# Kernel optimization log

Hardware: AMD Instinct MI355X
Metric: run time of the kernel (lower is better)

The kernel has to match this reference:

```python
import jax, jax.numpy as jnp
import numpy as np

B, S, HID = 2, 2048, 4096
NH, NKV, HD = 32, 8, 128
SLIDING_WINDOW = 1024
ROPE_THETA = 10000.0


def setup_inputs() -> dict:
    key = jax.random.key(0)
    ks = jax.random.split(key, 6)
    hidden_states = jax.random.normal(ks[0], (B, S, HID), dtype=jnp.float32)
    attention_mask = jnp.ones((B, S), dtype=jnp.int32)
    position_ids = jnp.broadcast_to(jnp.arange(S, dtype=jnp.int32)[None, :], (B, S))
    sc = 1.0 / np.sqrt(HID)
    q_w = jax.random.normal(ks[1], (HID, NH * HD), dtype=jnp.float32) * sc
    k_w = jax.random.normal(ks[2], (HID, NKV * HD), dtype=jnp.float32) * sc
    v_w = jax.random.normal(ks[3], (HID, NKV * HD), dtype=jnp.float32) * sc
    o_w = jax.random.normal(ks[4], (NH * HD, HID), dtype=jnp.float32) * sc
    return {"hidden_states": hidden_states, "attention_mask": attention_mask,
            "position_ids": position_ids, "q_w": q_w, "k_w": k_w, "v_w": v_w, "o_w": o_w}


def _rotate_half(x):
    return jnp.concatenate((-x[..., x.shape[-1] // 2:], x[..., : x.shape[-1] // 2]), axis=-1)


def _rope_sincos(position_ids):
    # inv_freq over even dims of head_dim; emb = concat(freqs, freqs)
    inv_freq = 1.0 / ROPE_THETA ** (jnp.arange(0, HD, 2, dtype=jnp.float32) / HD)
    freqs = position_ids.astype(jnp.float32)[..., None] * inv_freq  # [B,S,HD/2]
    emb = jnp.concatenate((freqs, freqs), axis=-1)                  # [B,S,HD]
    # broadcast over heads axis: [B,S,1,HD]
    return jnp.sin(emb)[:, :, None, :], jnp.cos(emb)[:, :, None, :]


def reference(hidden_states, attention_mask, position_ids, q_w, k_w, v_w, o_w):
    b, q_len, _ = hidden_states.shape
    n_rep = NH // NKV

    q = (hidden_states @ q_w).reshape(b, q_len, NH, HD)
    k = (hidden_states @ k_w).reshape(b, q_len, NKV, HD)
    v = (hidden_states @ v_w).reshape(b, q_len, NKV, HD)

    sin_pos, cos_pos = _rope_sincos(position_ids)
    q = q * cos_pos + _rotate_half(q) * sin_pos
    k = k * cos_pos + _rotate_half(k) * sin_pos

    # GQA: repeat kv heads (repeat_interleave along head axis)
    k = jnp.repeat(k, n_rep, axis=2)  # [B,S,NH,HD]
    v = jnp.repeat(v, n_rep, axis=2)

    # sliding-window causal mask: j <= i and j >= i - sliding_window
    i = jnp.arange(q_len)[:, None]
    j = jnp.arange(q_len)[None, :]
    band = (j <= i) & (j >= i - SLIDING_WINDOW)           # [Q,K]
    mask = band[None, None] & (attention_mask[:, None, None, :] > 0)  # [B,1,Q,K]

    bias = jnp.where(mask, 0.0, jnp.finfo(jnp.float32).min)

    scale = 1.0 / jnp.sqrt(jnp.asarray(HD, dtype=jnp.float32))
    scores = jnp.einsum('bqhd,bkhd->bhqk', q, k) * scale + bias
    attn_weights = jax.nn.softmax(scores, axis=-1)
    attn_out = jnp.einsum('bhqk,bkhd->bqhd', attn_weights, v)
    attn_out = attn_out.reshape(b, q_len, HID)
    return attn_out @ o_w
```

## Files before the change

### kernel.cpp

```cpp
#include <hip/hip_runtime.h>
#include <stdint.h>
#include <stddef.h>

typedef __bf16 bf16x8 __attribute__((ext_vector_type(8)));
typedef short short8 __attribute__((ext_vector_type(8)));
typedef float floatx4 __attribute__((ext_vector_type(4)));
typedef float f32x16 __attribute__((ext_vector_type(16)));
typedef unsigned short ushort4v __attribute__((ext_vector_type(4)));
typedef unsigned int uint2v __attribute__((ext_vector_type(2)));

__device__ __forceinline__ unsigned short f2bf(float f){
  unsigned int u = __float_as_uint(f);
  u += 0x7fffu + ((u >> 16) & 1u);
  return (unsigned short)(u >> 16);
}
__device__ __forceinline__ float bf2f(unsigned short s){
  return __uint_as_float(((unsigned int)s) << 16);
}
__device__ __forceinline__ void gl2lds16(const void* g, void* l){
  __builtin_amdgcn_global_load_lds((const __attribute__((address_space(1))) void*)g,
                                   (__attribute__((address_space(3))) void*)l, 16, 0, 0);
}

__global__ __launch_bounds__(256) void conv_f32_bf16(const float* __restrict__ in,
                                                     unsigned short* __restrict__ out){
  int t = blockIdx.x * 256 + threadIdx.x;
  floatx4 v = *(const floatx4*)(in + (size_t)t * 4);
  ushort4v o;
#pragma unroll
  for (int j = 0; j < 4; ++j) o[j] = f2bf(v[j]);
  *(ushort4v*)(out + (size_t)t * 4) = o;
}

__global__ __launch_bounds__(256) void transpose_cvt(const float* __restrict__ in,
                                                     unsigned short* __restrict__ out,
                                                     int Kd, int Nd){
  __shared__ __align__(16) unsigned short tile[64 * 80];
  int n0 = blockIdx.x * 64, k0 = blockIdx.y * 64;
  int t = threadIdx.x;
#pragma unroll
  for (int it = 0; it < 2; ++it){
    int rr = (t >> 3) + it * 32;
    int cc = t & 7;
    const float* src = in + (size_t)(k0 + rr) * Nd + n0 + cc * 8;
    floatx4 a = *(const floatx4*)src;
    floatx4 b = *(const floatx4*)(src + 4);
    short8 s;
#pragma unroll
    for (int j = 0; j < 4; ++j){ s[j] = (short)f2bf(a[j]); s[j + 4] = (short)f2bf(b[j]); }
    *(short8*)&tile[rr * 80 + cc * 8] = s;
  }
  __syncthreads();
#pragma unroll
  for (int it = 0; it < 2; ++it){
    int nr = (t >> 3) + it * 32;
    int kc = t & 7;
    short8 v;
#pragma unroll
    for (int j = 0; j < 8; ++j) v[j] = (short)tile[(kc * 8 + j) * 80 + nr];
    *(short8*)(out + (size_t)(n0 + nr) * Kd + k0 + kc * 8) = v;
  }
}

__global__ __launch_bounds__(256, 2) void gemm_bt(
    const unsigned short* __restrict__ A,
    const unsigned short* __restrict__ Wq,
    const unsigned short* __restrict__ Wk,
    const unsigned short* __restrict__ Wv,
    unsigned short* __restrict__ oQ,
    unsigned short* __restrict__ oK,
    unsigned short* __restrict__ oVt,
    float* __restrict__ oF, int f32out)
{
  __shared__ __align__(16) unsigned short As[128 * 64];
  __shared__ __align__(16) unsigned short Bs[128 * 64];
  const int tid = threadIdx.x;
  const int w = tid >> 6, lane = tid & 63, quad = lane >> 4, l15 = lane & 15;
  const int wm64 = (w >> 1) * 64, wn64 = (w & 1) * 64;
  const int m0 = blockIdx.y * 128;
  const int n0 = blockIdx.x * 128;

  const unsigned short* Wsrc;
  int nb, region;
  if (n0 < 4096)      { Wsrc = Wq; nb = n0;        region = 0; }
  else if (n0 < 5120) { Wsrc = Wk; nb = n0 - 4096; region = 1; }
  else                { Wsrc = Wv; nb = n0 - 5120; region = 2; }

  floatx4 acc[4][4];
#pragma unroll
  for (int i = 0; i < 4; ++i)
#pragma unroll
    for (int j = 0; j < 4; ++j) acc[i][j] = (floatx4){0.f, 0.f, 0.f, 0.f};

  const int rsub = lane >> 3, csub = lane & 7;

  for (int k0 = 0; k0 < 4096; k0 += 64){
#pragma unroll
    for (int i = 0; i < 4; ++i){
      int u = i * 4 + w;
      int r = u * 8 + rsub;
      gl2lds16(A    + ((size_t)(m0 + r) << 12) + k0 + ((csub ^ (r & 7)) << 3), (char*)As + u * 1024);
      gl2lds16(Wsrc + ((size_t)(nb + r) << 12) + k0 + ((csub ^ (r & 7)) << 3), (char*)Bs + u * 1024);
    }
    __syncthreads();
#pragma unroll
    for (int ks = 0; ks < 2; ++ks){
      bf16x8 af[4], bfr[4];
#pragma unroll
      for (int mt = 0; mt < 4; ++mt){
        int r = wm64 + mt * 16 + l15;
        int kc = ks * 4 + quad;
        af[mt] = *(const bf16x8*)&As[r * 64 + ((kc ^ (r & 7)) << 3)];
      }
#pragma unroll
      for (int nt = 0; nt < 4; ++nt){
        int r = wn64 + nt * 16 + l15;
        int kc = ks * 4 + quad;
        bfr[nt] = *(const bf16x8*)&Bs[r * 64 + ((kc ^ (r & 7)) << 3)];
      }
#pragma unroll
      for (int mt = 0; mt < 4; ++mt)
#pragma unroll
        for (int nt = 0; nt < 4; ++nt)
          acc[mt][nt] = __builtin_amdgcn_mfma_f32_16x16x32_bf16(af[mt], bfr[nt], acc[mt][nt], 0, 0, 0);
    }
    __syncthreads();
  }

  if (region == 0){
    if (f32out){
#pragma unroll
      for (int mt = 0; mt < 4; ++mt)
#pragma unroll
        for (int nt = 0; nt < 4; ++nt){
          int gn = n0 + wn64 + nt * 16 + l15;
#pragma unroll
          for (int rr = 0; rr < 4; ++rr){
            int gm = m0 + wm64 + mt * 16 + quad * 4 + rr;
            oF[((size_t)gm << 12) + gn] = acc[mt][nt][rr];
          }
        }
    } else {
#pragma unroll
      for (int mt = 0; mt < 4; ++mt)
#pragma unroll
        for (int nt = 0; nt < 4; ++nt){
          int gn = n0 + wn64 + nt * 16 + l15;
#pragma unroll
          for (int rr = 0; rr < 4; ++rr){
            int gm = m0 + wm64 + mt * 16 + quad * 4 + rr;
            oQ[((size_t)gm << 12) + gn] = f2bf(acc[mt][nt][rr]);
          }
        }
    }
  } else if (region == 1){
#pragma unroll
    for (int mt = 0; mt < 4; ++mt)
#pragma unroll
      for (int nt = 0; nt < 4; ++nt){
        int gn = n0 - 4096 + wn64 + nt * 16 + l15;
#pragma unroll
        for (int rr = 0; rr < 4; ++rr){
          int gm = m0 + wm64 + mt * 16 + quad * 4 + rr;
          oK[((size_t)gm << 10) + gn] = f2bf(acc[mt][nt][rr]);
        }
      }
  } else {
#pragma unroll
    for (int mt = 0; mt < 4; ++mt){
      int gm0 = m0 + wm64 + mt * 16 + quad * 4;
      int b = gm0 >> 11, s0 = gm0 & 2047;
#pragma unroll
      for (int nt = 0; nt < 4; ++nt){
        int dg = n0 - 5120 + wn64 + nt * 16 + l15;
        int kvh = dg >> 7, d = dg & 127;
        ushort4v pk;
#pragma unroll
        for (int rr = 0; rr < 4; ++rr) pk[rr] = f2bf(acc[mt][nt][rr]);
        *(ushort4v*)(oVt + (((size_t)(b * 8 + kvh) * 128 + d) * 2048 + s0)) = pk;
      }
    }
  }
}

__global__ void rope_apply_k(unsigned short* __restrict__ Qb, unsigned short* __restrict__ Kb,
                             const int* __restrict__ pos){
  int t = blockIdx.x * 256 + threadIdx.x;
  unsigned short* base;
  int row, ch;
  bool isq = (t < 1048576);
  if (isq){ row = t >> 8; int c = t & 255; base = Qb + ((size_t)row << 12) + (c >> 3) * 128; ch = c & 7; }
  else { int t2 = t - 1048576; row = t2 >> 6; int c = t2 & 63; base = Kb + ((size_t)row << 10) + (c >> 3) * 128; ch = c & 7; }
  float p = (float)pos[row];
  const float qs = 0.08838834764831845f * 1.44269504088896340736f;
  float sc_out = isq ? qs : 1.0f;
  int d0 = ch * 8;
  short8 x0 = *(short8*)(base + d0);
  short8 x1 = *(short8*)(base + d0 + 64);
  short8 y0, y1;
#pragma unroll
  for (int j = 0; j < 8; ++j){
    float ang = p * exp2f(-(float)(d0 + j) * 0.20762050593045952f);
    float sn = sinf(ang), cs = cosf(ang);
    float a  = bf2f((unsigned short)x0[j]);
    float bb = bf2f((unsigned short)x1[j]);
    y0[j] = (short)f2bf((a * cs - bb * sn) * sc_out);
    y1[j] = (short)f2bf((bb * cs + a * sn) * sc_out);
  }
  *(short8*)(base + d0)      = y0;
  *(short8*)(base + d0 + 64) = y1;
}

__global__ __launch_bounds__(256, 2) void flash_swa(
    const unsigned short* __restrict__ Q,
    const unsigned short* __restrict__ K,
    const unsigned short* __restrict__ Vt,
    const int* __restrict__ amask,
    unsigned short* __restrict__ attn)
{
  __shared__ __align__(16) unsigned short Kl[2][64 * 128];
  __shared__ __align__(16) unsigned short Vl[2][128 * 64];
  __shared__ __align__(16) unsigned int   Pl[4][1024];
  const int h = blockIdx.y, b = blockIdx.z;
  const int kv = h >> 2;
  const int tid = threadIdx.x, w = tid >> 6, lane = tid & 63;
  const int l31 = lane & 31, hi = lane >> 5, hi4 = hi << 2;
  const int qb = blockIdx.x * 128;
  const int t0 = qb >> 6;
  const int qw0 = qb + w * 32;
  const int aw = t0 + (w >> 1);

  bool anybad = false;
  {
    const int* ap = amask + b * 2048 + lane * 32;
#pragma unroll
    for (int i = 0; i < 8; ++i){
      int4 mv = *(const int4*)(ap + i * 4);
      anybad |= (mv.x <= 0) | (mv.y <= 0) | (mv.z <= 0) | (mv.w <= 0);
    }
  }
  const bool allv = (__ballot(anybad) == 0ull);

  bf16x8 qf[8];
  {
    const unsigned short* qbase = Q + (((size_t)(b * 2048 + qw0 + l31)) << 12) + h * 128;
#pragma unroll
    for (int ds = 0; ds < 8; ++ds) qf[ds] = *(const bf16x8*)(qbase + ds * 16 + hi * 8);
  }

  f32x16 acco[4];
#pragma unroll
  for (int i = 0; i < 4; ++i)
#pragma unroll
    for (int j = 0; j < 16; ++j) acco[i][j] = 0.f;
  float m_i = -1e30f, l_i = 0.f;

  const int jb0 = (t0 >= 16) ? (t0 - 16) : 0;
  const int jtend = t0 + 1;

#define STAGE_KV(JT, BUF)                                                                  \
  {                                                                                        \
    const int k0s = (JT) * 64;                                                             \
    _Pragma("unroll")                                                                      \
    for (int i_ = 0; i_ < 4; ++i_){                                                        \
      int u_ = i_ * 4 + w;                                                                 \
      int r_ = u_ * 4 + (lane >> 4);                                                       \
      int c_ = lane & 15;                                                                  \
      gl2lds16(K + (((size_t)(b * 2048 + k0s + r_)) << 10) + kv * 128 + ((c_ ^ (r_ & 15)) << 3), \
               (char*)Kl[BUF] + u_ * 1024);                                                \
    }                                                                                      \
    _Pragma("unroll")                                                                      \
    for (int i_ = 0; i_ < 4; ++i_){                                                        \
      int u_ = i_ * 4 + w;                                                                 \
      int d_ = u_ * 8 + (lane >> 3);                                                       \
      int c_ = lane & 7;                                                                   \
      gl2lds16(Vt + ((size_t)(b * 8 + kv) * 128 + d_) * 2048 + k0s + ((c_ ^ (d_ & 7)) << 3), \
               (char*)Vl[BUF] + u_ * 1024);                                                \
    }                                                                                      \
  }

  STAGE_KV(jb0, 0);
  __syncthreads();

  unsigned int* Pw = &Pl[w][0];
  int cur = 0;
  for (int jt = jb0; jt <= jtend; ++jt){
    if (jt < jtend) STAGE_KV(jt + 1, cur ^ 1);

    const bool active = (jt >= aw - 16) && (jt <= aw);
    if (active){
      const int k0 = jt * 64;
      const unsigned short* Klc = Kl[cur];
      const unsigned short* Vlc = Vl[cur];

      f32x16 ps[2];
#pragma unroll
      for (int kb = 0; kb < 2; ++kb)
#pragma unroll
        for (int j = 0; j < 16; ++j) ps[kb][j] = 0.f;

      __builtin_amdgcn_s_setprio(1);
#pragma unroll
      for (int ds = 0; ds < 8; ++ds){
#pragma unroll
        for (int kb = 0; kb < 2; ++kb){
          int r = kb * 32 + l31;
          bf16x8 kf = *(const bf16x8*)&Klc[r * 128 + (((ds * 2 + hi) ^ (r & 15)) << 3)];
          ps[kb] = __builtin_amdgcn_mfma_f32_32x32x16_bf16(kf, qf[ds], ps[kb], 0, 0, 0);
        }
      }
      __builtin_amdgcn_s_setprio(0);

      const bool slow = (jt == aw) || (jt == aw - 16) || (!allv);
      if (slow){
        unsigned long long mb = __ballot(amask[b * 2048 + k0 + lane] > 0);
        int irow = qw0 + l31;
#pragma unroll
        for (int kb = 0; kb < 2; ++kb)
#pragma unroll
          for (int reg = 0; reg < 16; ++reg){
            int jv = k0 + kb * 32 + (reg & 3) + 8 * (reg >> 2) + hi4;
            bool valid = (jv <= irow) && (jv >= irow - 1024) &&
                         (((mb >> (jv & 63)) & 1ull) != 0ull);
            ps[kb][reg] = valid ? ps[kb][reg] : -1e30f;
          }
      }

      float t16[16];
#pragma unroll
      for (int r = 0; r < 16; ++r) t16[r] = fmaxf(ps[0][r], ps[1][r]);
      float t8[8];
#pragma unroll
      for (int r = 0; r < 8; ++r) t8[r] = fmaxf(t16[r], t16[r + 8]);
      float t4[4];
#pragma unroll
      for (int r = 0; r < 4; ++r) t4[r] = fmaxf(t8[r], t8[r + 4]);
      float vm = fmaxf(fmaxf(t4[0], t4[1]), fmaxf(t4[2], t4[3]));
      float vmax = fmaxf(vm, __shfl_xor(vm, 32));

      if (!__all(vmax - m_i <= 8.0f)){
        float mnew = fmaxf(m_i, vmax);
        float alpha = exp2f(m_i - mnew);
        m_i = mnew;
        l_i *= alpha;
#pragma unroll
        for (int db = 0; db < 4; ++db) acco[db] *= alpha;
      }

#pragma unroll
      for (int kb = 0; kb < 2; ++kb)
#pragma unroll
        for (int reg = 0; reg < 16; ++reg) ps[kb][reg] = exp2f(ps[kb][reg] - m_i);

      float s16[16];
#pragma unroll
      for (int r = 0; r < 16; ++r) s16[r] = ps[0][r] + ps[1][r];
      float s8[8];
#pragma unroll
      for (int r = 0; r < 8; ++r) s8[r] = s16[r] + s16[r + 8];
      float s4[4];
#pragma unroll
      for (int r = 0; r < 4; ++r) s4[r] = s8[r] + s8[r + 4];
      float sm = (s4[0] + s4[1]) + (s4[2] + s4[3]);
      l_i += sm + __shfl_xor(sm, 32);

#pragma unroll
      for (int kb = 0; kb < 2; ++kb)
#pragma unroll
        for (int g = 0; g < 4; ++g){
          unsigned p0 = (unsigned)f2bf(ps[kb][g * 4 + 0]) | ((unsigned)f2bf(ps[kb][g * 4 + 1]) << 16);
          unsigned p1 = (unsigned)f2bf(ps[kb][g * 4 + 2]) | ((unsigned)f2bf(ps[kb][g * 4 + 3]) << 16);
          int ch = (kb * 4 + g) ^ (l31 & 7);
          uint2v pv_; pv_[0] = p0; pv_[1] = p1;
          *(uint2v*)&Pw[l31 * 32 + ch * 4 + hi * 2] = pv_;
        }
      bf16x8 pa[4];
#pragma unroll
      for (int ks = 0; ks < 4; ++ks)
        pa[ks] = *(const bf16x8*)&Pw[l31 * 32 + (((ks * 2 + hi) ^ (l31 & 7)) << 2)];

      __builtin_amdgcn_s_setprio(1);
#pragma unroll
      for (int ks = 0; ks < 4; ++ks){
#pragma unroll
        for (int db = 0; db < 4; ++db){
          int d = db * 32 + l31;
          bf16x8 vf = *(const bf16x8*)&Vlc[d * 64 + (((ks * 2 + hi) ^ (d & 7)) << 3)];
          acco[db] = __builtin_amdgcn_mfma_f32_32x32x16_bf16(vf, pa[ks], acco[db], 0, 0, 0);
        }
      }
      __builtin_amdgcn_s_setprio(0);
    }

    __syncthreads();
    cur ^= 1;
  }
#undef STAGE_KV

  float invl = 1.f / l_i;
  unsigned short* Ep = ((unsigned short*)Kl) + w * 4096;
  {
    const int q = l31;
#pragma unroll
    for (int db = 0; db < 4; ++db)
#pragma unroll
      for (int reg = 0; reg < 16; ++reg){
        int dc = db * 4 + (reg >> 2);
        int dl = (reg & 3) + hi4;
        Ep[q * 128 + ((dc ^ (q & 15)) << 3) + dl] = f2bf(acco[db][reg] * invl);
      }
  }
  {
    const int rr_ = lane >> 4, cc = lane & 15;
#pragma unroll
    for (int p8 = 0; p8 < 8; ++p8){
      int q = p8 * 4 + rr_;
      short8 vv = *(const short8*)&Ep[q * 128 + ((cc ^ (q & 15)) << 3)];
      size_t off = (((size_t)(b * 2048 + qb + w * 32 + q)) << 12) + h * 128 + cc * 8;
      *(short8*)(attn + off) = vv;
    }
  }
}

extern "C" void kernel_launch(void* const* d_in, const int* in_sizes, int n_in,
                              void* d_out, int out_size, void* d_ws, size_t ws_size,
                              hipStream_t stream){
  const float* hidden = (const float*)d_in[0];
  const int* amask = (const int*)d_in[1];
  const int* pos   = (const int*)d_in[2];
  const float* qw = (const float*)d_in[3];
  const float* kw = (const float*)d_in[4];
  const float* vw = (const float*)d_in[5];
  const float* ow = (const float*)d_in[6];

  char* ws = (char*)d_ws;
  unsigned short* hb   = (unsigned short*)(ws + 0);
  unsigned short* qt   = (unsigned short*)(ws + 33554432);
  unsigned short* kt   = (unsigned short*)(ws + 67108864);
  unsigned short* vtw  = (unsigned short*)(ws + 75497472);
  unsigned short* Qb   = (unsigned short*)(ws + 83886080);
  unsigned short* Kb   = (unsigned short*)(ws + 117440512);
  unsigned short* Vtb  = (unsigned short*)(ws + 125829120);
  unsigned short* ot   = hb;
  unsigned short* attn = qt;
  float* outp = (float*)d_out;

  hipLaunchKernelGGL(conv_f32_bf16, dim3(16384), dim3(256), 0, stream, hidden, hb);
  hipLaunchKernelGGL(transpose_cvt, dim3(64, 64), dim3(256), 0, stream, qw, qt, 4096, 4096);
  hipLaunchKernelGGL(transpose_cvt, dim3(16, 64), dim3(256), 0, stream, kw, kt, 4096, 1024);
  hipLaunchKernelGGL(transpose_cvt, dim3(16, 64), dim3(256), 0, stream, vw, vtw, 4096, 1024);
  hipLaunchKernelGGL(gemm_bt, dim3(48, 32), dim3(256), 0, stream,
                     hb, qt, kt, vtw, Qb, Kb, Vtb, (float*)nullptr, 0);
  hipLaunchKernelGGL(transpose_cvt, dim3(64, 64), dim3(256), 0, stream, ow, ot, 4096, 4096);
  hipLaunchKernelGGL(rope_apply_k, dim3(5120), dim3(256), 0, stream, Qb, Kb, pos);
  hipLaunchKernelGGL(flash_swa, dim3(16, 32, 2), dim3(256), 0, stream, Qb, Kb, Vtb, amask, attn);
  hipLaunchKernelGGL(gemm_bt, dim3(32, 32), dim3(256), 0, stream,
                     attn, ot, ot, ot, nullptr, nullptr, nullptr, outp, 1);
}
```

Measured before the change: 698.8 us.

## Rewrite projection GEMM as 256x256 tile, 8-wave, double-buffered LDS pipeline

Replaces the 128x128, 4-wave GEMM with 256x256 tiles computed by 8 waves. LDS is double-buffered so the async global-to-LDS loads for the next K step are interleaved with the MFMA quadrants of the current step. Partial vmcnt waits, barriers and s_setprio are used to overlap loads with compute. This raises data reuse per block and hides load latency, but uses 128KB of LDS and leaves fewer blocks in the grid (384 and 256), which can underfill the GPU.

```diff
diff --git a/kernel.cpp b/kernel.cpp
--- a/kernel.cpp
+++ b/kernel.cpp
@@ -62,7 +62,7 @@
   }
 }
 
-__global__ __launch_bounds__(256, 2) void gemm_bt(
+__global__ __launch_bounds__(512, 2) void gemm_bt(
     const unsigned short* __restrict__ A,
     const unsigned short* __restrict__ Wq,
     const unsigned short* __restrict__ Wk,
@@ -72,13 +72,13 @@
     unsigned short* __restrict__ oVt,
     float* __restrict__ oF, int f32out)
 {
-  __shared__ __align__(16) unsigned short As[128 * 64];
-  __shared__ __align__(16) unsigned short Bs[128 * 64];
+  __shared__ __align__(16) unsigned short As[2][256 * 64];
+  __shared__ __align__(16) unsigned short Bs[2][256 * 64];
   const int tid = threadIdx.x;
   const int w = tid >> 6, lane = tid & 63, quad = lane >> 4, l15 = lane & 15;
-  const int wm64 = (w >> 1) * 64, wn64 = (w & 1) * 64;
-  const int m0 = blockIdx.y * 128;
-  const int n0 = blockIdx.x * 128;
+  const int wr = w >> 2, wc = w & 3;
+  const int m0 = blockIdx.y * 256;
+  const int n0 = blockIdx.x * 256;
 
   const unsigned short* Wsrc;
   int nb, region;
@@ -86,97 +86,192 @@
   else if (n0 < 5120) { Wsrc = Wk; nb = n0 - 4096; region = 1; }
   else                { Wsrc = Wv; nb = n0 - 5120; region = 2; }
 
-  floatx4 acc[4][4];
-#pragma unroll
-  for (int i = 0; i < 4; ++i)
+  floatx4 acc[8][4];
+#pragma unroll
+  for (int i = 0; i < 8; ++i)
 #pragma unroll
     for (int j = 0; j < 4; ++j) acc[i][j] = (floatx4){0.f, 0.f, 0.f, 0.f};
 
-  const int rsub = lane >> 3, csub = lane & 7;
-
-  for (int k0 = 0; k0 < 4096; k0 += 64){
+#define STG(SRC, ROW0, H, DST, K0)                                                     \
+  { _Pragma("unroll")                                                                  \
+    for (int rep_ = 0; rep_ < 2; ++rep_){                                              \
+      int u_ = tid + rep_ * 512;                                                       \
+      int r_ = (H) * 128 + (u_ >> 3);                                                  \
+      int c_ = u_ & 7;                                                                 \
+      gl2lds16((SRC) + ((size_t)((ROW0) + r_) << 12) + (K0) + ((c_ ^ (r_ & 7)) << 3),  \
+               (char*)(DST) + (H) * 16384 + (size_t)u_ * 16);                          \
+    } }
+
+  STG(A,    m0, 0, &As[0][0], 0);
+  STG(Wsrc, nb, 0, &Bs[0][0], 0);
+  STG(Wsrc, nb, 1, &Bs[0][0], 0);
+  STG(A,    m0, 1, &As[0][0], 0);
+  asm volatile("s_waitcnt vmcnt(4)" ::: "memory");
+  __builtin_amdgcn_s_barrier();
+
+  for (int t = 0; t < 64; ++t){
+    const int cb = t & 1, nbuf = cb ^ 1;
+    const int s = (t < 63) ? (t + 1) : 63;
+    const int kn = s << 6;
+    const unsigned short* Ac = &As[cb][0];
+    const unsigned short* Bc = &Bs[cb][0];
+
+    bf16x8 af[4][2], bf0[2][2], bf1[2][2];
+
 #pragma unroll
     for (int i = 0; i < 4; ++i){
-      int u = i * 4 + w;
-      int r = u * 8 + rsub;
-      gl2lds16(A    + ((size_t)(m0 + r) << 12) + k0 + ((csub ^ (r & 7)) << 3), (char*)As + u * 1024);
-      gl2lds16(Wsrc + ((size_t)(nb + r) << 12) + k0 + ((csub ^ (r & 7)) << 3), (char*)Bs + u * 1024);
-    }
-    __syncthreads();
-#pragma unroll
-    for (int ks = 0; ks < 2; ++ks){
-      bf16x8 af[4], bfr[4];
-#pragma unroll
-      for (int mt = 0; mt < 4; ++mt){
-        int r = wm64 + mt * 16 + l15;
+      int r = (wr * 4 + i) * 16 + l15;
+#pragma unroll
+      for (int ks = 0; ks < 2; ++ks){
         int kc = ks * 4 + quad;
-        af[mt] = *(const bf16x8*)&As[r * 64 + ((kc ^ (r & 7)) << 3)];
-      }
-#pragma unroll
-      for (int nt = 0; nt < 4; ++nt){
-        int r = wn64 + nt * 16 + l15;
+        af[i][ks] = *(const bf16x8*)&Ac[r * 64 + ((kc ^ (r & 7)) << 3)];
+      }
+    }
+#pragma unroll
+    for (int j = 0; j < 2; ++j){
+      int r = (wc * 2 + j) * 16 + l15;
+#pragma unroll
+      for (int ks = 0; ks < 2; ++ks){
         int kc = ks * 4 + quad;
-        bfr[nt] = *(const bf16x8*)&Bs[r * 64 + ((kc ^ (r & 7)) << 3)];
-      }
-#pragma unroll
-      for (int mt = 0; mt < 4; ++mt)
-#pragma unroll
-        for (int nt = 0; nt < 4; ++nt)
-          acc[mt][nt] = __builtin_amdgcn_mfma_f32_16x16x32_bf16(af[mt], bfr[nt], acc[mt][nt], 0, 0, 0);
-    }
-    __syncthreads();
-  }
+        bf0[j][ks] = *(const bf16x8*)&Bc[r * 64 + ((kc ^ (r & 7)) << 3)];
+      }
+    }
+    STG(A, m0, 0, &As[nbuf][0], kn);
+    __builtin_amdgcn_s_setprio(1);
+#pragma unroll
+    for (int i = 0; i < 4; ++i)
+#pragma unroll
+      for (int j = 0; j < 2; ++j)
+#pragma unroll
+        for (int ks = 0; ks < 2; ++ks)
+          acc[i][j] = __builtin_amdgcn_mfma_f32_16x16x32_bf16(af[i][ks], bf0[j][ks], acc[i][j], 0, 0, 0);
+    __builtin_amdgcn_s_setprio(0);
+    asm volatile("s_waitcnt vmcnt(4)" ::: "memory");
+    __builtin_amdgcn_s_barrier();
+
+#pragma unroll
+    for (int j = 0; j < 2; ++j){
+      int r = (8 + wc * 2 + j) * 16 + l15;
+#pragma unroll
+      for (int ks = 0; ks < 2; ++ks){
+        int kc = ks * 4 + quad;
+        bf1[j][ks] = *(const bf16x8*)&Bc[r * 64 + ((kc ^ (r & 7)) << 3)];
+      }
+    }
+    STG(Wsrc, nb, 0, &Bs[nbuf][0], kn);
+    __builtin_amdgcn_s_setprio(1);
+#pragma unroll
+    for (int i = 0; i < 4; ++i)
+#pragma unroll
+      for (int j = 0; j < 2; ++j)
+#pragma unroll
+        for (int ks = 0; ks < 2; ++ks)
+          acc[i][2 + j] = __builtin_amdgcn_mfma_f32_16x16x32_bf16(af[i][ks], bf1[j][ks], acc[i][2 + j], 0, 0, 0);
+    __builtin_amdgcn_s_setprio(0);
+    asm volatile("s_waitcnt vmcnt(4)" ::: "memory");
+    __builtin_amdgcn_s_barrier();
+
+#pragma unroll
+    for (int i = 0; i < 4; ++i){
+      int r = (8 + wr * 4 + i) * 16 + l15;
+#pragma unroll
+      for (int ks = 0; ks < 2; ++ks){
+        int kc = ks * 4 + quad;
+        af[i][ks] = *(const bf16x8*)&Ac[r * 64 + ((kc ^ (r & 7)) << 3)];
+      }
+    }
+    STG(Wsrc, nb, 1, &Bs[nbuf][0], kn);
+    __builtin_amdgcn_s_setprio(1);
+#pragma unroll
+    for (int i = 0; i < 4; ++i)
+#pragma unroll
+      for (int j = 0; j < 2; ++j)
+#pragma unroll
+        for (int ks = 0; ks < 2; ++ks)
+          acc[4 + i][2 + j] = __builtin_amdgcn_mfma_f32_16x16x32_bf16(af[i][ks], bf1[j][ks], acc[4 + i][2 + j], 0, 0, 0);
+    __builtin_amdgcn_s_setprio(0);
+    __builtin_amdgcn_s_barrier();
+
+#pragma unroll
+    for (int j = 0; j < 2; ++j){
+      int r = (wc * 2 + j) * 16 + l15;
+#pragma unroll
+      for (int ks = 0; ks < 2; ++ks){
+        int kc = ks * 4 + quad;
+        bf0[j][ks] = *(const bf16x8*)&Bc[r * 64 + ((kc ^ (r & 7)) << 3)];
+      }
+    }
+    STG(A, m0, 1, &As[nbuf][0], kn);
+    __builtin_amdgcn_s_setprio(1);
+#pragma unroll
+    for (int i = 0; i < 4; ++i)
+#pragma unroll
+      for (int j = 0; j < 2; ++j)
+#pragma unroll
+        for (int ks = 0; ks < 2; ++ks)
+          acc[4 + i][j] = __builtin_amdgcn_mfma_f32_16x16x32_bf16(af[i][ks], bf0[j][ks], acc[4 + i][j], 0, 0, 0);
+    __builtin_amdgcn_s_setprio(0);
+    asm volatile("s_waitcnt vmcnt(4)" ::: "memory");
+    __builtin_amdgcn_s_barrier();
+  }
+#undef STG
 
   if (region == 0){
     if (f32out){
 #pragma unroll
-      for (int mt = 0; mt < 4; ++mt)
-#pragma unroll
-        for (int nt = 0; nt < 4; ++nt){
-          int gn = n0 + wn64 + nt * 16 + l15;
+      for (int mi = 0; mi < 8; ++mi){
+        const int row = (mi >> 2) * 128 + wr * 64 + (mi & 3) * 16 + quad * 4;
+#pragma unroll
+        for (int nj = 0; nj < 4; ++nj){
+          const int gn = n0 + (nj >> 1) * 128 + wc * 32 + (nj & 1) * 16 + l15;
 #pragma unroll
           for (int rr = 0; rr < 4; ++rr){
-            int gm = m0 + wm64 + mt * 16 + quad * 4 + rr;
-            oF[((size_t)gm << 12) + gn] = acc[mt][nt][rr];
+            const int gm = m0 + row + rr;
+            oF[((size_t)gm << 12) + gn] = acc[mi][nj][rr];
           }
         }
+      }
     } else {
 #pragma unroll
-      for (int mt = 0; mt < 4; ++mt)
-#pragma unroll
-        for (int nt = 0; nt < 4; ++nt){
-          int gn = n0 + wn64 + nt * 16 + l15;
+      for (int mi = 0; mi < 8; ++mi){
+        const int row = (mi >> 2) * 128 + wr * 64 + (mi & 3) * 16 + quad * 4;
+#pragma unroll
+        for (int nj = 0; nj < 4; ++nj){
+          const int gn = n0 + (nj >> 1) * 128 + wc * 32 + (nj & 1) * 16 + l15;
 #pragma unroll
           for (int rr = 0; rr < 4; ++rr){
-            int gm = m0 + wm64 + mt * 16 + quad * 4 + rr;
-            oQ[((size_t)gm << 12) + gn] = f2bf(acc[mt][nt][rr]);
+            const int gm = m0 + row + rr;
+            oQ[((size_t)gm << 12) + gn] = f2bf(acc[mi][nj][rr]);
           }
         }
+      }
     }
   } else if (region == 1){
 #pragma unroll
-    for (int mt = 0; mt < 4; ++mt)
-#pragma unroll
-      for (int nt = 0; nt < 4; ++nt){
-        int gn = n0 - 4096 + wn64 + nt * 16 + l15;
+    for (int mi = 0; mi < 8; ++mi){
+      const int row = (mi >> 2) * 128 + wr * 64 + (mi & 3) * 16 + quad * 4;
+#pragma unroll
+      for (int nj = 0; nj < 4; ++nj){
+        const int gn = n0 - 4096 + (nj >> 1) * 128 + wc * 32 + (nj & 1) * 16 + l15;
 #pragma unroll
         for (int rr = 0; rr < 4; ++rr){
-          int gm = m0 + wm64 + mt * 16 + quad * 4 + rr;
-          oK[((size_t)gm << 10) + gn] = f2bf(acc[mt][nt][rr]);
+          const int gm = m0 + row + rr;
+          oK[((size_t)gm << 10) + gn] = f2bf(acc[mi][nj][rr]);
         }
       }
+    }
   } else {
 #pragma unroll
-    for (int mt = 0; mt < 4; ++mt){
-      int gm0 = m0 + wm64 + mt * 16 + quad * 4;
-      int b = gm0 >> 11, s0 = gm0 & 2047;
-#pragma unroll
-      for (int nt = 0; nt < 4; ++nt){
-        int dg = n0 - 5120 + wn64 + nt * 16 + l15;
-        int kvh = dg >> 7, d = dg & 127;
+    for (int mi = 0; mi < 8; ++mi){
+      const int gm0 = m0 + (mi >> 2) * 128 + wr * 64 + (mi & 3) * 16 + quad * 4;
+      const int b = gm0 >> 11, s0 = gm0 & 2047;
+#pragma unroll
+      for (int nj = 0; nj < 4; ++nj){
+        const int dg = n0 - 5120 + (nj >> 1) * 128 + wc * 32 + (nj & 1) * 16 + l15;
+        const int kvh = dg >> 7, d = dg & 127;
         ushort4v pk;
 #pragma unroll
-        for (int rr = 0; rr < 4; ++rr) pk[rr] = f2bf(acc[mt][nt][rr]);
+        for (int rr = 0; rr < 4; ++rr) pk[rr] = f2bf(acc[mi][nj][rr]);
         *(ushort4v*)(oVt + (((size_t)(b * 8 + kvh) * 128 + d) * 2048 + s0)) = pk;
       }
     }
@@ -449,11 +544,11 @@
   hipLaunchKernelGGL(transpose_cvt, dim3(64, 64), dim3(256), 0, stream, qw, qt, 4096, 4096);
   hipLaunchKernelGGL(transpose_cvt, dim3(16, 64), dim3(256), 0, stream, kw, kt, 4096, 1024);
   hipLaunchKernelGGL(transpose_cvt, dim3(16, 64), dim3(256), 0, stream, vw, vtw, 4096, 1024);
-  hipLaunchKernelGGL(gemm_bt, dim3(48, 32), dim3(256), 0, stream,
+  hipLaunchKernelGGL(gemm_bt, dim3(24, 16), dim3(512), 0, stream,
                      hb, qt, kt, vtw, Qb, Kb, Vtb, (float*)nullptr, 0);
   hipLaunchKernelGGL(transpose_cvt, dim3(64, 64), dim3(256), 0, stream, ow, ot, 4096, 4096);
   hipLaunchKernelGGL(rope_apply_k, dim3(5120), dim3(256), 0, stream, Qb, Kb, pos);
   hipLaunchKernelGGL(flash_swa, dim3(16, 32, 2), dim3(256), 0, stream, Qb, Kb, Vtb, amask, attn);
-  hipLaunchKernelGGL(gemm_bt, dim3(32, 32), dim3(256), 0, stream,
+  hipLaunchKernelGGL(gemm_bt, dim3(16, 16), dim3(512), 0, stream,
                      attn, ot, ot, ot, nullptr, nullptr, nullptr, outp, 1);
 }
```

Result: no change. 699.8 us (+0.1%).

## Replace GEMM with 256x256-tile, 8-wave, double-buffered pipelined kernel

Applied to the files above, without the earlier changes.

Rewrites the projection GEMM as a 512-thread kernel computing 256x256 output tiles. Global-to-LDS loads are double-buffered and interleaved with MFMA phases using barriers, s_setprio and explicit vmcnt waits. This is meant to hide load latency and raise data reuse per tile. The cost is a much larger LDS footprint (128KB per block) and fewer blocks in the grid.

```diff
diff --git a/kernel.cpp b/kernel.cpp
--- a/kernel.cpp
+++ b/kernel.cpp
@@ -62,7 +62,7 @@
   }
 }
 
-__global__ __launch_bounds__(256, 2) void gemm_bt(
+__global__ __launch_bounds__(512, 2) void gemm8(
     const unsigned short* __restrict__ A,
     const unsigned short* __restrict__ Wq,
     const unsigned short* __restrict__ Wk,
@@ -72,13 +72,13 @@
     unsigned short* __restrict__ oVt,
     float* __restrict__ oF, int f32out)
 {
-  __shared__ __align__(16) unsigned short As[128 * 64];
-  __shared__ __align__(16) unsigned short Bs[128 * 64];
+  __shared__ __align__(16) unsigned short As[2][256 * 64];
+  __shared__ __align__(16) unsigned short Bs[2][256 * 64];
   const int tid = threadIdx.x;
   const int w = tid >> 6, lane = tid & 63, quad = lane >> 4, l15 = lane & 15;
-  const int wm64 = (w >> 1) * 64, wn64 = (w & 1) * 64;
-  const int m0 = blockIdx.y * 128;
-  const int n0 = blockIdx.x * 128;
+  const int wr = w >> 2, wc = w & 3;
+  const int m0 = blockIdx.y * 256;
+  const int n0 = blockIdx.x * 256;
 
   const unsigned short* Wsrc;
   int nb, region;
@@ -86,100 +86,181 @@
   else if (n0 < 5120) { Wsrc = Wk; nb = n0 - 4096; region = 1; }
   else                { Wsrc = Wv; nb = n0 - 5120; region = 2; }
 
-  floatx4 acc[4][4];
-#pragma unroll
-  for (int i = 0; i < 4; ++i)
-#pragma unroll
-    for (int j = 0; j < 4; ++j) acc[i][j] = (floatx4){0.f, 0.f, 0.f, 0.f};
-
-  const int rsub = lane >> 3, csub = lane & 7;
-
-  for (int k0 = 0; k0 < 4096; k0 += 64){
-#pragma unroll
-    for (int i = 0; i < 4; ++i){
-      int u = i * 4 + w;
-      int r = u * 8 + rsub;
-      gl2lds16(A    + ((size_t)(m0 + r) << 12) + k0 + ((csub ^ (r & 7)) << 3), (char*)As + u * 1024);
-      gl2lds16(Wsrc + ((size_t)(nb + r) << 12) + k0 + ((csub ^ (r & 7)) << 3), (char*)Bs + u * 1024);
-    }
-    __syncthreads();
-#pragma unroll
-    for (int ks = 0; ks < 2; ++ks){
-      bf16x8 af[4], bfr[4];
-#pragma unroll
-      for (int mt = 0; mt < 4; ++mt){
-        int r = wm64 + mt * 16 + l15;
-        int kc = ks * 4 + quad;
-        af[mt] = *(const bf16x8*)&As[r * 64 + ((kc ^ (r & 7)) << 3)];
-      }
-#pragma unroll
-      for (int nt = 0; nt < 4; ++nt){
-        int r = wn64 + nt * 16 + l15;
-        int kc = ks * 4 + quad;
-        bfr[nt] = *(const bf16x8*)&Bs[r * 64 + ((kc ^ (r & 7)) << 3)];
-      }
-#pragma unroll
-      for (int mt = 0; mt < 4; ++mt)
-#pragma unroll
-        for (int nt = 0; nt < 4; ++nt)
-          acc[mt][nt] = __builtin_amdgcn_mfma_f32_16x16x32_bf16(af[mt], bfr[nt], acc[mt][nt], 0, 0, 0);
-    }
-    __syncthreads();
-  }
+  floatx4 acc[2][4][2][2];
+#pragma unroll
+  for (int a_ = 0; a_ < 2; ++a_)
+#pragma unroll
+    for (int b_ = 0; b_ < 4; ++b_)
+#pragma unroll
+      for (int c_ = 0; c_ < 2; ++c_)
+#pragma unroll
+        for (int d_ = 0; d_ < 2; ++d_) acc[a_][b_][c_][d_] = (floatx4){0.f, 0.f, 0.f, 0.f};
+
+#define STG(SRC, ROW0, H, DST, K0)                                                     \
+  { _Pragma("unroll")                                                                  \
+    for (int rep_ = 0; rep_ < 2; ++rep_){                                              \
+      int u_ = tid + rep_ * 512;                                                       \
+      int r_ = (H) * 128 + (u_ >> 3);                                                  \
+      int c_ = u_ & 7;                                                                 \
+      gl2lds16((SRC) + ((size_t)((ROW0) + r_) << 12) + (K0) + ((c_ ^ (r_ & 7)) << 3),  \
+               (char*)(DST) + (H) * 16384 + (size_t)u_ * 16);                          \
+    } }
+
+#define READA(BUF, MH)                                                                 \
+  { _Pragma("unroll")                                                                  \
+    for (int mt = 0; mt < 4; ++mt){                                                    \
+      int r = (MH) * 128 + wr * 64 + mt * 16 + l15;                                    \
+      _Pragma("unroll")                                                                \
+      for (int ks = 0; ks < 2; ++ks){                                                  \
+        int kc = ks * 4 + quad;                                                        \
+        af[mt][ks] = *(const bf16x8*)&(BUF)[r * 64 + ((kc ^ (r & 7)) << 3)];           \
+      } } }
+
+#define READB(BUF, NH)                                                                 \
+  { _Pragma("unroll")                                                                  \
+    for (int nt = 0; nt < 2; ++nt){                                                    \
+      int r = (NH) * 128 + wc * 32 + nt * 16 + l15;                                    \
+      _Pragma("unroll")                                                                \
+      for (int ks = 0; ks < 2; ++ks){                                                  \
+        int kc = ks * 4 + quad;                                                        \
+        bfr[nt][ks] = *(const bf16x8*)&(BUF)[r * 64 + ((kc ^ (r & 7)) << 3)];          \
+      } } }
+
+#define MFMACL(MH, NH)                                                                 \
+  { _Pragma("unroll")                                                                  \
+    for (int mt = 0; mt < 4; ++mt)                                                     \
+      _Pragma("unroll")                                                                \
+      for (int nt = 0; nt < 2; ++nt)                                                   \
+        _Pragma("unroll")                                                              \
+        for (int ks = 0; ks < 2; ++ks)                                                 \
+          acc[MH][mt][NH][nt] = __builtin_amdgcn_mfma_f32_16x16x32_bf16(               \
+              af[mt][ks], bfr[nt][ks], acc[MH][mt][NH][nt], 0, 0, 0); }
+
+#define PH(RA, MH, RB, NH, ABUF, BBUF, STGSTMT, VM)                                    \
+  { if (RA) READA(ABUF, MH);                                                           \
+    if (RB) READB(BBUF, NH);                                                           \
+    STGSTMT;                                                                           \
+    asm volatile("" ::: "memory");                                                     \
+    __builtin_amdgcn_s_barrier();                                                      \
+    __builtin_amdgcn_s_setprio(1);                                                     \
+    MFMACL(MH, NH);                                                                    \
+    __builtin_amdgcn_s_setprio(0);                                                     \
+    if (VM) asm volatile("s_waitcnt vmcnt(4)" ::: "memory");                           \
+    asm volatile("" ::: "memory");                                                     \
+    __builtin_amdgcn_s_barrier(); }
+
+  STG(A,    m0, 0, &As[0][0], 0);
+  STG(Wsrc, nb, 0, &Bs[0][0], 0);
+  STG(Wsrc, nb, 1, &Bs[0][0], 0);
+  STG(A,    m0, 1, &As[0][0], 0);
+  STG(Wsrc, nb, 0, &Bs[1][0], 64);
+  STG(A,    m0, 1, &As[1][0], 64);
+  asm volatile("s_waitcnt vmcnt(4)" ::: "memory");
+  asm volatile("" ::: "memory");
+  __builtin_amdgcn_s_barrier();
+
+  for (int i = 0; i < 32; ++i){
+    const int k1 = (2 * i + 1) << 6;
+    const int t2 = 2 * i + 2, t3 = 2 * i + 3;
+    const int k2 = (t2 < 64 ? t2 : 63) << 6;
+    const int k3 = (t3 < 64 ? t3 : 63) << 6;
+    const unsigned short* A0p = &As[0][0];
+    const unsigned short* B0p = &Bs[0][0];
+    const unsigned short* A1p = &As[1][0];
+    const unsigned short* B1p = &Bs[1][0];
+    bf16x8 af[4][2], bfr[2][2];
+
+    PH(1, 0, 1, 0, A0p, B0p, STG(A,    m0, 0, &As[1][0], k1), 0)
+    PH(1, 1, 0, 0, A0p, B0p, STG(Wsrc, nb, 1, &Bs[1][0], k1), 0)
+    PH(0, 1, 1, 1, A0p, B0p, STG(Wsrc, nb, 0, &Bs[0][0], k2), 0)
+    PH(1, 0, 0, 1, A0p, B0p, STG(A,    m0, 1, &As[0][0], k2), 1)
+    PH(1, 0, 1, 0, A1p, B1p, STG(A,    m0, 0, &As[0][0], k2), 0)
+    PH(1, 1, 0, 0, A1p, B1p, STG(Wsrc, nb, 1, &Bs[0][0], k2), 0)
+    PH(0, 1, 1, 1, A1p, B1p, STG(Wsrc, nb, 0, &Bs[1][0], k3), 0)
+    PH(1, 0, 0, 1, A1p, B1p, STG(A,    m0, 1, &As[1][0], k3), 1)
+  }
+  asm volatile("s_waitcnt vmcnt(0)" ::: "memory");
+#undef PH
+#undef MFMACL
+#undef READB
+#undef READA
+#undef STG
 
   if (region == 0){
     if (f32out){
 #pragma unroll
-      for (int mt = 0; mt < 4; ++mt)
-#pragma unroll
-        for (int nt = 0; nt < 4; ++nt){
-          int gn = n0 + wn64 + nt * 16 + l15;
-#pragma unroll
-          for (int rr = 0; rr < 4; ++rr){
-            int gm = m0 + wm64 + mt * 16 + quad * 4 + rr;
-            oF[((size_t)gm << 12) + gn] = acc[mt][nt][rr];
-          }
+      for (int mh = 0; mh < 2; ++mh)
+#pragma unroll
+        for (int mt = 0; mt < 4; ++mt){
+          const int row = mh * 128 + wr * 64 + mt * 16 + quad * 4;
+#pragma unroll
+          for (int nh = 0; nh < 2; ++nh)
+#pragma unroll
+            for (int nt = 0; nt < 2; ++nt){
+              const int gn = n0 + nh * 128 + wc * 32 + nt * 16 + l15;
+#pragma unroll
+              for (int rr = 0; rr < 4; ++rr){
+                const int gm = m0 + row + rr;
+                oF[((size_t)gm << 12) + gn] = acc[mh][mt][nh][nt][rr];
+              }
+            }
         }
     } else {
 #pragma unroll
-      for (int mt = 0; mt < 4; ++mt)
-#pragma unroll
-        for (int nt = 0; nt < 4; ++nt){
-          int gn = n0 + wn64 + nt * 16 + l15;
-#pragma unroll
-          for (int rr = 0; rr < 4; ++rr){
-            int gm = m0 + wm64 + mt * 16 + quad * 4 + rr;
-            oQ[((size_t)gm << 12) + gn] = f2bf(acc[mt][nt][rr]);
-          }
+      for (int mh = 0; mh < 2; ++mh)
+#pragma unroll
+        for (int mt = 0; mt < 4; ++mt){
+          const int row = mh * 128 + wr * 64 + mt * 16 + quad * 4;
+#pragma unroll
+          for (int nh = 0; nh < 2; ++nh)
+#pragma unroll
+            for (int nt = 0; nt < 2; ++nt){
+              const int gn = n0 + nh * 128 + wc * 32 + nt * 16 + l15;
+#pragma unroll
+              for (int rr = 0; rr < 4; ++rr){
+                const int gm = m0 + row + rr;
+                oQ[((size_t)gm << 12) + gn] = f2bf(acc[mh][mt][nh][nt][rr]);
+              }
+            }
         }
     }
   } else if (region == 1){
 #pragma unroll
-    for (int mt = 0; mt < 4; ++mt)
-#pragma unroll
-      for (int nt = 0; nt < 4; ++nt){
-        int gn = n0 - 4096 + wn64 + nt * 16 + l15;
-#pragma unroll
-        for (int rr = 0; rr < 4; ++rr){
-          int gm = m0 + wm64 + mt * 16 + quad * 4 + rr;
-          oK[((size_t)gm << 10) + gn] = f2bf(acc[mt][nt][rr]);
-        }
+    for (int mh = 0; mh < 2; ++mh)
+#pragma unroll
+      for (int mt = 0; mt < 4; ++mt){
+        const int row = mh * 128 + wr * 64 + mt * 16 + quad * 4;
+#pragma unroll
+        for (int nh = 0; nh < 2; ++nh)
+#pragma unroll
+          for (int nt = 0; nt < 2; ++nt){
+            const int gn = n0 - 4096 + nh * 128 + wc * 32 + nt * 16 + l15;
+#pragma unroll
+            for (int rr = 0; rr < 4; ++rr){
+              const int gm = m0 + row + rr;
+              oK[((size_t)gm << 10) + gn] = f2bf(acc[mh][mt][nh][nt][rr]);
+            }
+          }
       }
   } else {
 #pragma unroll
-    for (int mt = 0; mt < 4; ++mt){
-      int gm0 = m0 + wm64 + mt * 16 + quad * 4;
-      int b = gm0 >> 11, s0 = gm0 & 2047;
-#pragma unroll
-      for (int nt = 0; nt < 4; ++nt){
-        int dg = n0 - 5120 + wn64 + nt * 16 + l15;
-        int kvh = dg >> 7, d = dg & 127;
-        ushort4v pk;
-#pragma unroll
-        for (int rr = 0; rr < 4; ++rr) pk[rr] = f2bf(acc[mt][nt][rr]);
-        *(ushort4v*)(oVt + (((size_t)(b * 8 + kvh) * 128 + d) * 2048 + s0)) = pk;
-      }
-    }
+    for (int mh = 0; mh < 2; ++mh)
+#pragma unroll
+      for (int mt = 0; mt < 4; ++mt){
+        const int gm0 = m0 + mh * 128 + wr * 64 + mt * 16 + quad * 4;
+        const int b = gm0 >> 11, s0 = gm0 & 2047;
+#pragma unroll
+        for (int nh = 0; nh < 2; ++nh)
+#pragma unroll
+          for (int nt = 0; nt < 2; ++nt){
+            const int dg = n0 - 5120 + nh * 128 + wc * 32 + nt * 16 + l15;
+            const int kvh = dg >> 7, d = dg & 127;
+            ushort4v pk;
+#pragma unroll
+            for (int rr = 0; rr < 4; ++rr) pk[rr] = f2bf(acc[mh][mt][nh][nt][rr]);
+            *(ushort4v*)(oVt + (((size_t)(b * 8 + kvh) * 128 + d) * 2048 + s0)) = pk;
+          }
+      }
   }
 }
 
@@ -449,11 +530,11 @@
   hipLaunchKernelGGL(transpose_cvt, dim3(64, 64), dim3(256), 0, stream, qw, qt, 4096, 4096);
   hipLaunchKernelGGL(transpose_cvt, dim3(16, 64), dim3(256), 0, stream, kw, kt, 4096, 1024);
   hipLaunchKernelGGL(transpose_cvt, dim3(16, 64), dim3(256), 0, stream, vw, vtw, 4096, 1024);
-  hipLaunchKernelGGL(gemm_bt, dim3(48, 32), dim3(256), 0, stream,
+  hipLaunchKernelGGL(gemm8, dim3(24, 16), dim3(512), 0, stream,
                      hb, qt, kt, vtw, Qb, Kb, Vtb, (float*)nullptr, 0);
   hipLaunchKernelGGL(transpose_cvt, dim3(64, 64), dim3(256), 0, stream, ow, ot, 4096, 4096);
   hipLaunchKernelGGL(rope_apply_k, dim3(5120), dim3(256), 0, stream, Qb, Kb, pos);
   hipLaunchKernelGGL(flash_swa, dim3(16, 32, 2), dim3(256), 0, stream, Qb, Kb, Vtb, amask, attn);
-  hipLaunchKernelGGL(gemm_bt, dim3(32, 32), dim3(256), 0, stream,
+  hipLaunchKernelGGL(gemm8, dim3(16, 16), dim3(512), 0, stream,
                      attn, ot, ot, ot, nullptr, nullptr, nullptr, outp, 1);
 }
```

Measured after the change: 756.8 us. +8.3%, slower.

## Fuse RoPE into QKV GEMM epilogue and merge prep conversion kernels

Applied to the files above, without the earlier changes.

The standalone RoPE kernel, which re-read and re-wrote Q and K in bf16 while computing sin/cos per element, is removed. RoPE is now applied in the QKV GEMM epilogue: partner halves are exchanged through LDS and sin/cos come from a small precomputed table stored temporarily in the output buffer. The hidden-state conversion and three weight-transpose kernels are merged into one launch. This trades a separate memory pass and launch overhead for extra syncs and LDS traffic in the epilogue; rounding also changes slightly because RoPE now works on fp32 accumulators.

```diff
diff --git a/kernel.cpp b/kernel.cpp
--- a/kernel.cpp
+++ b/kernel.cpp
@@ -9,6 +9,8 @@
 typedef unsigned short ushort4v __attribute__((ext_vector_type(4)));
 typedef unsigned int uint2v __attribute__((ext_vector_type(2)));
 
+#define QSCALE 0.12753785471843077f
+
 __device__ __forceinline__ unsigned short f2bf(float f){
   unsigned int u = __float_as_uint(f);
   u += 0x7fffu + ((u >> 16) & 1u);
@@ -22,22 +24,11 @@
                                    (__attribute__((address_space(3))) void*)l, 16, 0, 0);
 }
 
-__global__ __launch_bounds__(256) void conv_f32_bf16(const float* __restrict__ in,
-                                                     unsigned short* __restrict__ out){
-  int t = blockIdx.x * 256 + threadIdx.x;
-  floatx4 v = *(const floatx4*)(in + (size_t)t * 4);
-  ushort4v o;
-#pragma unroll
-  for (int j = 0; j < 4; ++j) o[j] = f2bf(v[j]);
-  *(ushort4v*)(out + (size_t)t * 4) = o;
-}
-
-__global__ __launch_bounds__(256) void transpose_cvt(const float* __restrict__ in,
-                                                     unsigned short* __restrict__ out,
-                                                     int Kd, int Nd){
-  __shared__ __align__(16) unsigned short tile[64 * 80];
-  int n0 = blockIdx.x * 64, k0 = blockIdx.y * 64;
-  int t = threadIdx.x;
+__device__ __forceinline__ void transpose_body(const float* __restrict__ in,
+                                               unsigned short* __restrict__ out,
+                                               int Kd, int Nd, int bx, int by, int t,
+                                               unsigned short* tile){
+  int n0 = bx * 64, k0 = by * 64;
 #pragma unroll
   for (int it = 0; it < 2; ++it){
     int rr = (t >> 3) + it * 32;
@@ -62,7 +53,53 @@
   }
 }
 
-__global__ __launch_bounds__(256, 2) void gemm_bt(
+__global__ __launch_bounds__(256) void transpose_cvt(const float* __restrict__ in,
+                                                     unsigned short* __restrict__ out,
+                                                     int Kd, int Nd){
+  __shared__ __align__(16) unsigned short tile[64 * 80];
+  transpose_body(in, out, Kd, Nd, blockIdx.x, blockIdx.y, threadIdx.x, tile);
+}
+
+__global__ __launch_bounds__(256) void prep_fused(const float* __restrict__ hidden,
+                                                  unsigned short* __restrict__ hb,
+                                                  const float* __restrict__ qw,
+                                                  unsigned short* __restrict__ qtw,
+                                                  const float* __restrict__ kw,
+                                                  unsigned short* __restrict__ kt,
+                                                  const float* __restrict__ vw,
+                                                  unsigned short* __restrict__ vtw){
+  __shared__ __align__(16) unsigned short tile[64 * 80];
+  const int bid = blockIdx.x, t = threadIdx.x;
+  if (bid < 16384){
+    int i = bid * 256 + t;
+    floatx4 v = *(const floatx4*)(hidden + (size_t)i * 4);
+    ushort4v o;
+#pragma unroll
+    for (int j = 0; j < 4; ++j) o[j] = f2bf(v[j]);
+    *(ushort4v*)(hb + (size_t)i * 4) = o;
+  } else if (bid < 20480){
+    int b2 = bid - 16384;
+    transpose_body(qw, qtw, 4096, 4096, b2 & 63, b2 >> 6, t, tile);
+  } else if (bid < 21504){
+    int b2 = bid - 20480;
+    transpose_body(kw, kt, 4096, 1024, b2 & 15, b2 >> 4, t, tile);
+  } else {
+    int b2 = bid - 21504;
+    transpose_body(vw, vtw, 4096, 1024, b2 & 15, b2 >> 4, t, tile);
+  }
+}
+
+__global__ __launch_bounds__(256) void rope_table(const int* __restrict__ pos,
+                                                  float2* __restrict__ tab){
+  int t = blockIdx.x * 256 + threadIdx.x;
+  int row = t >> 6, dh = t & 63;
+  float p = (float)pos[row];
+  float ang = p * exp2f(-(float)dh * 0.20762050593045952f);
+  float2 sc; sc.x = sinf(ang); sc.y = cosf(ang);
+  tab[t] = sc;
+}
+
+__global__ __launch_bounds__(256, 2) void gemm_bt128(
     const unsigned short* __restrict__ A,
     const unsigned short* __restrict__ Wq,
     const unsigned short* __restrict__ Wk,
@@ -70,7 +107,8 @@
     unsigned short* __restrict__ oQ,
     unsigned short* __restrict__ oK,
     unsigned short* __restrict__ oVt,
-    float* __restrict__ oF, int f32out)
+    float* __restrict__ oF, int f32out,
+    const float2* __restrict__ rtab)
 {
   __shared__ __align__(16) unsigned short As[128 * 64];
   __shared__ __align__(16) unsigned short Bs[128 * 64];
@@ -127,44 +165,70 @@
     __syncthreads();
   }
 
-  if (region == 0){
-    if (f32out){
-#pragma unroll
-      for (int mt = 0; mt < 4; ++mt)
-#pragma unroll
-        for (int nt = 0; nt < 4; ++nt){
-          int gn = n0 + wn64 + nt * 16 + l15;
-#pragma unroll
-          for (int rr = 0; rr < 4; ++rr){
-            int gm = m0 + wm64 + mt * 16 + quad * 4 + rr;
-            oF[((size_t)gm << 12) + gn] = acc[mt][nt][rr];
-          }
-        }
-    } else {
-#pragma unroll
-      for (int mt = 0; mt < 4; ++mt)
-#pragma unroll
-        for (int nt = 0; nt < 4; ++nt){
-          int gn = n0 + wn64 + nt * 16 + l15;
-#pragma unroll
-          for (int rr = 0; rr < 4; ++rr){
-            int gm = m0 + wm64 + mt * 16 + quad * 4 + rr;
-            oQ[((size_t)gm << 12) + gn] = f2bf(acc[mt][nt][rr]);
-          }
-        }
+  if (region == 0 && f32out){
+#pragma unroll
+    for (int mt = 0; mt < 4; ++mt)
+#pragma unroll
+      for (int nt = 0; nt < 4; ++nt){
+        int gn = n0 + wn64 + nt * 16 + l15;
+#pragma unroll
+        for (int rr = 0; rr < 4; ++rr){
+          int gm = m0 + wm64 + mt * 16 + quad * 4 + rr;
+          oF[((size_t)gm << 12) + gn] = acc[mt][nt][rr];
+        }
+      }
+  } else if (region == 0){
+    float* Ex = (float*)As;
+#pragma unroll
+    for (int mt = 0; mt < 4; ++mt){
+      __syncthreads();
+#pragma unroll
+      for (int nt = 0; nt < 4; ++nt)
+#pragma unroll
+        for (int rr = 0; rr < 4; ++rr)
+          Ex[((w * 4 + nt) * 4 + rr) * 64 + lane] = acc[mt][nt][rr];
+      __syncthreads();
+#pragma unroll
+      for (int nt = 0; nt < 4; ++nt){
+        int d = wn64 + nt * 16 + l15;
+        int dh = d & 63;
+#pragma unroll
+        for (int rr = 0; rr < 4; ++rr){
+          int gm = m0 + wm64 + mt * 16 + quad * 4 + rr;
+          float2 sc = rtab[gm * 64 + dh];
+          float x  = acc[mt][nt][rr];
+          float xp = Ex[(((w ^ 1) * 4 + nt) * 4 + rr) * 64 + lane];
+          float y = (d < 64) ? (x * sc.y - xp * sc.x) : (x * sc.y + xp * sc.x);
+          oQ[((size_t)gm << 12) + n0 + d] = f2bf(y * QSCALE);
+        }
+      }
     }
   } else if (region == 1){
-#pragma unroll
-    for (int mt = 0; mt < 4; ++mt)
+    float* Ex = (float*)As;
+#pragma unroll
+    for (int mt = 0; mt < 4; ++mt){
+      __syncthreads();
+#pragma unroll
+      for (int nt = 0; nt < 4; ++nt)
+#pragma unroll
+        for (int rr = 0; rr < 4; ++rr)
+          Ex[((w * 4 + nt) * 4 + rr) * 64 + lane] = acc[mt][nt][rr];
+      __syncthreads();
 #pragma unroll
       for (int nt = 0; nt < 4; ++nt){
         int gn = n0 - 4096 + wn64 + nt * 16 + l15;
+        int dh = gn & 63;
 #pragma unroll
         for (int rr = 0; rr < 4; ++rr){
           int gm = m0 + wm64 + mt * 16 + quad * 4 + rr;
-          oK[((size_t)gm << 10) + gn] = f2bf(acc[mt][nt][rr]);
-        }
-      }
+          float2 sc = rtab[gm * 64 + dh];
+          float x  = acc[mt][nt][rr];
+          float xp = Ex[(((w ^ 1) * 4 + nt) * 4 + rr) * 64 + lane];
+          float y = ((gn & 64) == 0) ? (x * sc.y - xp * sc.x) : (x * sc.y + xp * sc.x);
+          oK[((size_t)gm << 10) + gn] = f2bf(y);
+        }
+      }
+    }
   } else {
 #pragma unroll
     for (int mt = 0; mt < 4; ++mt){
@@ -181,34 +245,6 @@
       }
     }
   }
-}
-
-__global__ void rope_apply_k(unsigned short* __restrict__ Qb, unsigned short* __restrict__ Kb,
-                             const int* __restrict__ pos){
-  int t = blockIdx.x * 256 + threadIdx.x;
-  unsigned short* base;
-  int row, ch;
-  bool isq = (t < 1048576);
-  if (isq){ row = t >> 8; int c = t & 255; base = Qb + ((size_t)row << 12) + (c >> 3) * 128; ch = c & 7; }
-  else { int t2 = t - 1048576; row = t2 >> 6; int c = t2 & 63; base = Kb + ((size_t)row << 10) + (c >> 3) * 128; ch = c & 7; }
-  float p = (float)pos[row];
-  const float qs = 0.08838834764831845f * 1.44269504088896340736f;
-  float sc_out = isq ? qs : 1.0f;
-  int d0 = ch * 8;
-  short8 x0 = *(short8*)(base + d0);
-  short8 x1 = *(short8*)(base + d0 + 64);
-  short8 y0, y1;
-#pragma unroll
-  for (int j = 0; j < 8; ++j){
-    float ang = p * exp2f(-(float)(d0 + j) * 0.20762050593045952f);
-    float sn = sinf(ang), cs = cosf(ang);
-    float a  = bf2f((unsigned short)x0[j]);
-    float bb = bf2f((unsigned short)x1[j]);
-    y0[j] = (short)f2bf((a * cs - bb * sn) * sc_out);
-    y1[j] = (short)f2bf((bb * cs + a * sn) * sc_out);
-  }
-  *(short8*)(base + d0)      = y0;
-  *(short8*)(base + d0 + 64) = y1;
 }
 
 __global__ __launch_bounds__(256, 2) void flash_swa(
@@ -444,16 +480,15 @@
   unsigned short* ot   = hb;
   unsigned short* attn = qt;
   float* outp = (float*)d_out;
-
-  hipLaunchKernelGGL(conv_f32_bf16, dim3(16384), dim3(256), 0, stream, hidden, hb);
-  hipLaunchKernelGGL(transpose_cvt, dim3(64, 64), dim3(256), 0, stream, qw, qt, 4096, 4096);
-  hipLaunchKernelGGL(transpose_cvt, dim3(16, 64), dim3(256), 0, stream, kw, kt, 4096, 1024);
-  hipLaunchKernelGGL(transpose_cvt, dim3(16, 64), dim3(256), 0, stream, vw, vtw, 4096, 1024);
-  hipLaunchKernelGGL(gemm_bt, dim3(48, 32), dim3(256), 0, stream,
-                     hb, qt, kt, vtw, Qb, Kb, Vtb, (float*)nullptr, 0);
+  float2* rtab = (float2*)d_out;
+
+  hipLaunchKernelGGL(prep_fused, dim3(22528), dim3(256), 0, stream,
+                     hidden, hb, qw, qt, kw, kt, vw, vtw);
+  hipLaunchKernelGGL(rope_table, dim3(1024), dim3(256), 0, stream, pos, rtab);
+  hipLaunchKernelGGL(gemm_bt128, dim3(48, 32), dim3(256), 0, stream,
+                     hb, qt, kt, vtw, Qb, Kb, Vtb, (float*)nullptr, 0, rtab);
   hipLaunchKernelGGL(transpose_cvt, dim3(64, 64), dim3(256), 0, stream, ow, ot, 4096, 4096);
-  hipLaunchKernelGGL(rope_apply_k, dim3(5120), dim3(256), 0, stream, Qb, Kb, pos);
   hipLaunchKernelGGL(flash_swa, dim3(16, 32, 2), dim3(256), 0, stream, Qb, Kb, Vtb, amask, attn);
-  hipLaunchKernelGGL(gemm_bt, dim3(32, 32), dim3(256), 0, stream,
-                     attn, ot, ot, ot, nullptr, nullptr, nullptr, outp, 1);
-}
+  hipLaunchKernelGGL(gemm_bt128, dim3(32, 32), dim3(256), 0, stream,
+                     attn, ot, ot, ot, nullptr, nullptr, nullptr, outp, 1, rtab);
+}
```

New measurement: 729.9 us. 4.4% more time.
